# Kernel optimization log

Hardware: AMD Instinct MI355X
Metric: run time of the kernel (lower is better)

The kernel has to match this reference:

```python
import jax, jax.numpy as jnp
import numpy as np

FP16_HUGE = 65504.0  # large additive mask constant (fp16-max style, as in AF2 torch ports)

B, N, T = 1, 384, 4
CQ, CT = 128, 64      # query (pair) channels, template pair channels
H = 4                 # num heads
D = CT // H           # per-head key/value dim = 16 (AF2: key_dim=value_dim=64 split over 4 heads)


def setup_inputs() -> dict:
    key = jax.random.key(0)
    ks = jax.random.split(key, 8)
    inp = {
        "query_embedding": jax.random.normal(ks[0], (B, N, N, CQ), jnp.float32),
        "template_pair_representation": jax.random.normal(ks[1], (B, T, N, N, CT), jnp.float32),
        "template_mask": jnp.ones((B, T), jnp.float32),
        # attention params (gating=False for template pointwise attention in AF2)
        "query_w": jax.random.normal(ks[2], (H, CQ, D), jnp.float32) * (CQ ** -0.5),
        "key_w": jax.random.normal(ks[3], (H, CT, D), jnp.float32) * (CT ** -0.5),
        "value_w": jax.random.normal(ks[4], (H, CT, D), jnp.float32) * (CT ** -0.5),
        "output_w": jax.random.normal(ks[5], (H, D, CQ), jnp.float32) * ((H * D) ** -0.5),
        "output_b": jnp.zeros((CQ,), jnp.float32),
    }
    return inp


def reference(query_embedding, template_pair_representation, template_mask,
              query_w, key_w, value_w, output_w, output_b):
    b, n, _, cq = query_embedding.shape
    t = template_mask.shape[-1]
    d = query_w.shape[-1]

    # [b, n*n, 1, cq]: each (i,j) pair position attends over templates
    flat_q = query_embedding.reshape(b, n * n, 1, cq)
    # [b, t, n, n, ct] -> [b, n, n, t, ct] -> [b, n*n, t, ct]
    flat_t = jnp.transpose(template_pair_representation, (0, 2, 3, 1, 4)).reshape(b, n * n, t, -1)

    # additive bias over key axis: 0 where mask=1, -FP16_HUGE where mask=0; [b,1,1,1,t]
    bias = FP16_HUGE * (template_mask[:, None, None, None, :] - 1.0)

    q = jnp.einsum('bpic,hcd->bphid', flat_q, query_w) * (d ** -0.5)  # [b,p,h,1,d]
    k = jnp.einsum('bptc,hcd->bphtd', flat_t, key_w)                  # [b,p,h,t,d]
    v = jnp.einsum('bptc,hcd->bphtd', flat_t, value_w)

    logits = jnp.einsum('bphid,bphtd->bphit', q, k) + bias            # [b,p,h,1,t]
    weights = jax.nn.softmax(logits, axis=-1)
    wv = jnp.einsum('bphit,bphtd->bphid', weights, v)                 # [b,p,h,1,d]
    out = jnp.einsum('bphid,hdc->bpic', wv, output_w) + output_b      # [b,p,1,cq]

    embedding = out.reshape(b, n, n, cq)
    tmask = (jnp.sum(template_mask.reshape(b, -1), axis=1) > 0.0).astype(embedding.dtype)
    return embedding * tmask[:, None, None, None]
```

## Files before the change

### kernel.cpp

```cpp
#include <hip/hip_runtime.h>
#include <hip/hip_bf16.h>

typedef __attribute__((ext_vector_type(8))) short bf16x8;
typedef __attribute__((ext_vector_type(4))) float f32x4;
typedef unsigned int u32;
typedef unsigned short u16;

#define NPOS 147456
#define NTILES 9216
#define NBLK 1536
#define ITERS 6

__device__ inline u16 bfc(float f) {
  union { __hip_bfloat16 h; u16 s; } u;
  u.h = __float2bfloat16(f);
  return u.s;
}

__global__ void prep_kernel(const float* __restrict__ wq, const float* __restrict__ wk,
                            const float* __restrict__ wv, const float* __restrict__ wo,
                            u16* __restrict__ wsf) {
  int gid = blockIdx.x * 256 + threadIdx.x;
  int idx, which;
  if (gid < 8192)       { idx = gid;         which = 0; }
  else if (gid < 12288) { idx = gid - 8192;  which = 1; }
  else if (gid < 16384) { idx = gid - 12288; which = 2; }
  else                  { idx = gid - 16384; which = 3; }
  int fragid = idx >> 9, lane = (idx >> 3) & 63, e = idx & 7;
  int l15 = lane & 15, g = lane >> 4;
  float v;
  if (which == 0) {
    int n = fragid >> 2, kc = fragid & 3;
    int c = kc * 32 + g * 8 + e;
    v = wq[n * 2048 + c * 16 + l15] * 0.25f;
  } else if (which == 1) {
    int n = fragid >> 1, kc = fragid & 1;
    int c = kc * 32 + g * 8 + e;
    v = wk[n * 1024 + c * 16 + l15];
  } else if (which == 2) {
    int n = fragid >> 1, kc = fragid & 1;
    int c = kc * 32 + g * 8 + e;
    v = wv[n * 1024 + c * 16 + l15];
  } else {
    int n8 = fragid >> 1, kc = fragid & 1;
    int hd = kc * 32 + g * 8 + e;
    v = wo[(hd >> 4) * 2048 + (hd & 15) * 128 + n8 * 16 + l15];
  }
  wsf[gid] = bfc(v);
}

#define WQF(n, kc)  ((((n) * 4 + (kc))) * 64)
#define WKF(n, kc)  ((16 + (n) * 2 + (kc)) * 64)
#define WVF(n, kc)  ((24 + (n) * 2 + (kc)) * 64)
#define WOF(n8, kc) ((32 + (n8) * 2 + (kc)) * 64)

typedef const __attribute__((address_space(1))) u32 gas_u32;
typedef __attribute__((address_space(3))) u32 las_u32;

#define STR2_(x) #x
#define WAITVM(n) asm volatile("s_waitcnt vmcnt(" STR2_(n) ")" ::: "memory")
#define SBAR      __builtin_amdgcn_s_barrier()
#define SCHB      __builtin_amdgcn_sched_barrier(0)
#define WAITLGKM  asm volatile("s_waitcnt lgkmcnt(0)" ::: "memory")

__global__ __launch_bounds__(256) void tpa_kernel(
    const float* __restrict__ qe, const float* __restrict__ tpr,
    const float* __restrict__ tmk_p, const float* __restrict__ ob,
    const u16* __restrict__ wsf, float* __restrict__ out)
{
  __shared__ int4 qls4[512];
  __shared__ int4 thA4[512];
  __shared__ int4 thB4[512];
  __shared__ u32 wvsh32[512];
  char* const qls  = (char*)qls4;
  char* const thA  = (char*)thA4;
  char* const thB  = (char*)thB4;
  char* const wvsh = (char*)wvsh32;

  const int tid = threadIdx.x;
  const int wid = tid >> 6;
  const int lane = tid & 63;
  const int l15 = lane & 15, g = lane >> 4;
  const int swz = (l15 & 7) << 4;
  const int h = wid;

  const char* qdb[2];
  #pragma unroll
  for (int j = 0; j < 2; ++j) {
    int m = (wid * 2 + j) * 64 + lane;
    int pos = m >> 5, c16 = m & 31;
    qdb[j] = (const char*)qe + (size_t)pos * 512 + ((c16 * 16) ^ ((pos & 7) << 4));
  }
  const char* tdb[2][2];
  #pragma unroll
  for (int hf = 0; hf < 2; ++hf)
    #pragma unroll
    for (int j = 0; j < 2; ++j) {
      int m = (wid * 2 + j) * 64 + lane;
      int t = hf * 2 + (m >> 8), pos = (m >> 4) & 15, c16 = m & 15;
      tdb[hf][j] = (const char*)tpr + ((size_t)t * NPOS + pos) * 256 +
                   ((c16 * 16) ^ ((pos & 7) << 4));
    }

#define STAGE_Q(P)                                                             \
  { _Pragma("unroll") for (int j = 0; j < 2; ++j) {                            \
      const char* s_ = qdb[j] + (size_t)(P) * 512;                             \
      char* d_ = qls + (wid * 2 + j) * 1024;                                   \
      __builtin_amdgcn_global_load_lds((gas_u32*)s_, (las_u32*)d_, 16, 0, 0); } }

#define STAGE_T(HF, DST, P)                                                    \
  { _Pragma("unroll") for (int j = 0; j < 2; ++j) {                            \
      const char* s_ = tdb[HF][j] + (size_t)(P) * 256;                         \
      char* d_ = (DST) + (wid * 2 + j) * 1024;                                 \
      __builtin_amdgcn_global_load_lds((gas_u32*)s_, (las_u32*)d_, 16, 0, 0); } }

  const bf16x8* wf = (const bf16x8*)wsf;
  bf16x8 wqf[4], wkf[2], wvf[2], wof[2][2];
  #pragma unroll
  for (int kc = 0; kc < 4; ++kc) wqf[kc] = wf[WQF(h, kc) + lane];
  #pragma unroll
  for (int kc = 0; kc < 2; ++kc) {
    wkf[kc] = wf[WKF(h, kc) + lane];
    wvf[kc] = wf[WVF(h, kc) + lane];
    wof[0][kc] = wf[WOF(2 * h + 0, kc) + lane];
    wof[1][kc] = wf[WOF(2 * h + 1, kc) + lane];
  }

  const float m0 = tmk_p[0], m1 = tmk_p[1], m2 = tmk_p[2], m3 = tmk_p[3];
  const float biasv[4] = {65504.0f * (m0 - 1.0f), 65504.0f * (m1 - 1.0f),
                          65504.0f * (m2 - 1.0f), 65504.0f * (m3 - 1.0f)};
  const float tmk = (m0 + m1 + m2 + m3 > 0.0f) ? 1.0f : 0.0f;

  f32x4 obf[2];
  {
    const f32x4* obase = reinterpret_cast<const f32x4*>(ob);
    #pragma unroll
    for (int j = 0; j < 2; ++j) {
      const f32x4 o = obase[(2 * h + j) * 4 + g];
      #pragma unroll
      for (int r = 0; r < 4; ++r) obf[j][r] = o[r] * tmk;
    }
  }

  SCHB;
  STAGE_Q(blockIdx.x * 16)
  STAGE_T(0, thA, blockIdx.x * 16)
  STAGE_T(1, thB, blockIdx.x * 16)
  SCHB;

#define TSTEP(TROW, BIAS)                                                      \
  { bf16x8 at0, at1;                                                           \
    { f32x4 lo = *(const f32x4*)((TROW) + ((g * 32) ^ swz));                   \
      f32x4 hi = *(const f32x4*)((TROW) + ((g * 32 + 16) ^ swz));              \
      _Pragma("unroll")                                                        \
      for (int e = 0; e < 4; ++e) { at0[e] = (short)bfc(lo[e]); at0[e + 4] = (short)bfc(hi[e]); } } \
    { f32x4 lo = *(const f32x4*)((TROW) + ((128 + g * 32) ^ swz));             \
      f32x4 hi = *(const f32x4*)((TROW) + ((128 + g * 32 + 16) ^ swz));        \
      _Pragma("unroll")                                                        \
      for (int e = 0; e < 4; ++e) { at1[e] = (short)bfc(lo[e]); at1[e + 4] = (short)bfc(hi[e]); } } \
    f32x4 kT = (f32x4){0.f, 0.f, 0.f, 0.f};                                    \
    f32x4 vT = (f32x4){0.f, 0.f, 0.f, 0.f};                                    \
    kT = __builtin_amdgcn_mfma_f32_16x16x32_bf16(wkf[0], at0, kT, 0, 0, 0);    \
    kT = __builtin_amdgcn_mfma_f32_16x16x32_bf16(wkf[1], at1, kT, 0, 0, 0);    \
    vT = __builtin_amdgcn_mfma_f32_16x16x32_bf16(wvf[0], at0, vT, 0, 0, 0);    \
    vT = __builtin_amdgcn_mfma_f32_16x16x32_bf16(wvf[1], at1, vT, 0, 0, 0);    \
    float lg = qT[0] * kT[0] + qT[1] * kT[1] + qT[2] * kT[2] + qT[3] * kT[3];  \
    lg += __shfl_xor(lg, 16);                                                  \
    lg += __shfl_xor(lg, 32);                                                  \
    const float w = __expf(lg + (BIAS));                                       \
    ssum += w;                                                                 \
    _Pragma("unroll")                                                          \
    for (int r = 0; r < 4; ++r) wvT[r] += w * vT[r]; }

#define BODY(IT, WNA)                                                          \
{                                                                              \
  const int it_ = (IT);                                                        \
  const int p0 = (blockIdx.x + it_ * NBLK) * 16;                               \
  const int np0 = (blockIdx.x + ((it_ + 1 < ITERS) ? it_ + 1 : it_) * NBLK) * 16; \
                                                    \
  SCHB; WAITVM(WNA); SBAR; SCHB;                                               \
  f32x4 qT = (f32x4){0.f, 0.f, 0.f, 0.f};                                      \
  { const char* qrow = qls + l15 * 512;                                        \
    _Pragma("unroll")                                                          \
    for (int kc = 0; kc < 4; ++kc) {                                           \
      const int cb = kc * 128 + g * 32;                                        \
      f32x4 lo = *(const f32x4*)(qrow + ((cb) ^ swz));                         \
      f32x4 hi = *(const f32x4*)(qrow + ((cb + 16) ^ swz));                    \
      bf16x8 aq;                                                               \
      _Pragma("unroll")                                                        \
      for (int e = 0; e < 4; ++e) { aq[e] = (short)bfc(lo[e]); aq[e + 4] = (short)bfc(hi[e]); } \
      qT = __builtin_amdgcn_mfma_f32_16x16x32_bf16(wqf[kc], aq, qT, 0, 0, 0);  \
    } }                                                                        \
  float ssum = 0.f;                                                            \
  f32x4 wvT = (f32x4){0.f, 0.f, 0.f, 0.f};                                     \
  TSTEP(thA + 0 * 4096 + l15 * 256, biasv[0])                                  \
  TSTEP(thA + 1 * 4096 + l15 * 256, biasv[1])                                  \
                                 \
  SCHB; WAITLGKM; SBAR; SCHB;                                                  \
  STAGE_Q(np0)                                                                 \
  STAGE_T(0, thA, np0)                                                         \
                                                        \
  SCHB; WAITVM(4); SBAR; SCHB;                                                 \
  TSTEP(thB + 0 * 4096 + l15 * 256, biasv[2])                                  \
  TSTEP(thB + 1 * 4096 + l15 * 256, biasv[3])                                  \
  { const float inv = tmk / fmaxf(ssum, 1e-30f);                               \
    u32 pk0 = (u32)bfc(wvT[0] * inv) | ((u32)bfc(wvT[1] * inv) << 16);         \
    u32 pk1 = (u32)bfc(wvT[2] * inv) | ((u32)bfc(wvT[3] * inv) << 16);         \
    const int hb = h * 32 + g * 8;                                             \
    *(u32*)(wvsh + ((l15 * 128 + hb) ^ swz))     = pk0;                        \
    *(u32*)(wvsh + ((l15 * 128 + hb + 4) ^ swz)) = pk1; }                      \
                                             \
  SCHB; WAITLGKM; SBAR; SCHB;                                                  \
  { bf16x8 bwv0 = *(const bf16x8*)(wvsh + ((l15 * 128 + g * 16)      ^ swz));  \
    bf16x8 bwv1 = *(const bf16x8*)(wvsh + ((l15 * 128 + 64 + g * 16) ^ swz));  \
    _Pragma("unroll")                                                          \
    for (int j = 0; j < 2; ++j) {                                              \
      f32x4 acc = (f32x4){0.f, 0.f, 0.f, 0.f};                                 \
      acc = __builtin_amdgcn_mfma_f32_16x16x32_bf16(wof[j][0], bwv0, acc, 0, 0, 0); \
      acc = __builtin_amdgcn_mfma_f32_16x16x32_bf16(wof[j][1], bwv1, acc, 0, 0, 0); \
      f32x4 res;                                                               \
      _Pragma("unroll")                                                        \
      for (int r = 0; r < 4; ++r) res[r] = acc[r] + obf[j][r];                 \
      *(f32x4*)(out + (size_t)(p0 + l15) * 128 + (2 * h + j) * 16 + g * 4) = res; \
    } }                                                                        \
  SCHB;                                                                        \
  STAGE_T(1, thB, np0)                                                         \
  SCHB;                                                                        \
}

  BODY(0, 2)
  #pragma unroll 1
  for (int it = 1; it < ITERS; ++it) {
    BODY(it, 4)
  }
}

extern "C" void kernel_launch(void* const* d_in, const int* in_sizes, int n_in,
                              void* d_out, int out_size, void* d_ws, size_t ws_size,
                              hipStream_t stream) {
  const float* qe  = (const float*)d_in[0];
  const float* tpr = (const float*)d_in[1];
  const float* tmk = (const float*)d_in[2];
  const float* wq  = (const float*)d_in[3];
  const float* wk  = (const float*)d_in[4];
  const float* wv  = (const float*)d_in[5];
  const float* wo  = (const float*)d_in[6];
  const float* ob  = (const float*)d_in[7];
  float* out = (float*)d_out;
  u16* wsf = (u16*)d_ws;

  prep_kernel<<<96, 256, 0, stream>>>(wq, wk, wv, wo, wsf);
  tpa_kernel<<<NBLK, 256, 0, stream>>>(qe, tpr, tmk, ob, wsf, out);
}
```

Before: 61.53 us.

## Process two 16-position tiles per block iteration and halve the grid

Each block now handles two 16-position tiles per iteration with duplicated LDS buffers, interleaving their Q GEMMs, template steps and output GEMMs. The grid is halved so each block covers 32 positions per iteration with the same iteration count. The aim is to amortize barriers and waits over twice the work and to expose more independent MFMA and load work for latency hiding. In exchange LDS use per block doubles, register pressure rises, and fewer blocks are resident, which may lower occupancy.

```diff
diff --git a/kernel.cpp b/kernel.cpp
--- a/kernel.cpp
+++ b/kernel.cpp
@@ -8,7 +8,7 @@
 
 #define NPOS 147456
 #define NTILES 9216
-#define NBLK 1536
+#define NBLK 768
 #define ITERS 6
 
 __device__ inline u16 bfc(float f) {
@@ -68,14 +68,14 @@
     const float* __restrict__ tmk_p, const float* __restrict__ ob,
     const u16* __restrict__ wsf, float* __restrict__ out)
 {
-  __shared__ int4 qls4[512];
-  __shared__ int4 thA4[512];
-  __shared__ int4 thB4[512];
-  __shared__ u32 wvsh32[512];
-  char* const qls  = (char*)qls4;
-  char* const thA  = (char*)thA4;
-  char* const thB  = (char*)thB4;
-  char* const wvsh = (char*)wvsh32;
+  __shared__ int4 qls4[2][512];
+  __shared__ int4 thA4[2][512];
+  __shared__ int4 thB4[2][512];
+  __shared__ u32 wvsh32[2][512];
+  char* const qls0 = (char*)qls4[0];   char* const qls1 = (char*)qls4[1];
+  char* const thA0 = (char*)thA4[0];   char* const thA1 = (char*)thA4[1];
+  char* const thB0 = (char*)thB4[0];   char* const thB1 = (char*)thB4[1];
+  char* const exc0 = (char*)wvsh32[0]; char* const exc1 = (char*)wvsh32[1];
 
   const int tid = threadIdx.x;
   const int wid = tid >> 6;
@@ -102,10 +102,10 @@
                    ((c16 * 16) ^ ((pos & 7) << 4));
     }
 
-#define STAGE_Q(P)                                                             \
+#define STAGE_Q(DST, P)                                                        \
   { _Pragma("unroll") for (int j = 0; j < 2; ++j) {                            \
       const char* s_ = qdb[j] + (size_t)(P) * 512;                             \
-      char* d_ = qls + (wid * 2 + j) * 1024;                                   \
+      char* d_ = (DST) + (wid * 2 + j) * 1024;                                 \
       __builtin_amdgcn_global_load_lds((gas_u32*)s_, (las_u32*)d_, 16, 0, 0); } }
 
 #define STAGE_T(HF, DST, P)                                                    \
@@ -143,12 +143,28 @@
   }
 
   SCHB;
-  STAGE_Q(blockIdx.x * 16)
-  STAGE_T(0, thA, blockIdx.x * 16)
-  STAGE_T(1, thB, blockIdx.x * 16)
+  STAGE_Q(qls0, blockIdx.x * 32)
+  STAGE_T(0, thA0, blockIdx.x * 32)
+  STAGE_Q(qls1, blockIdx.x * 32 + 16)
+  STAGE_T(0, thA1, blockIdx.x * 32 + 16)
+  STAGE_T(1, thB0, blockIdx.x * 32)
+  STAGE_T(1, thB1, blockIdx.x * 32 + 16)
   SCHB;
 
-#define TSTEP(TROW, BIAS)                                                      \
+#define QGEMM(QT, QBUF)                                                        \
+  { const char* qrow = (QBUF) + l15 * 512;                                     \
+    _Pragma("unroll")                                                          \
+    for (int kc = 0; kc < 4; ++kc) {                                           \
+      const int cb = kc * 128 + g * 32;                                        \
+      f32x4 lo = *(const f32x4*)(qrow + ((cb) ^ swz));                         \
+      f32x4 hi = *(const f32x4*)(qrow + ((cb + 16) ^ swz));                    \
+      bf16x8 aq;                                                               \
+      _Pragma("unroll")                                                        \
+      for (int e = 0; e < 4; ++e) { aq[e] = (short)bfc(lo[e]); aq[e + 4] = (short)bfc(hi[e]); } \
+      QT = __builtin_amdgcn_mfma_f32_16x16x32_bf16(wqf[kc], aq, QT, 0, 0, 0);  \
+    } }
+
+#define TSTEP(TROW, BIAS, QT, SSUM, WVT)                                       \
   { bf16x8 at0, at1;                                                           \
     { f32x4 lo = *(const f32x4*)((TROW) + ((g * 32) ^ swz));                   \
       f32x4 hi = *(const f32x4*)((TROW) + ((g * 32 + 16) ^ swz));              \
@@ -164,55 +180,25 @@
     kT = __builtin_amdgcn_mfma_f32_16x16x32_bf16(wkf[1], at1, kT, 0, 0, 0);    \
     vT = __builtin_amdgcn_mfma_f32_16x16x32_bf16(wvf[0], at0, vT, 0, 0, 0);    \
     vT = __builtin_amdgcn_mfma_f32_16x16x32_bf16(wvf[1], at1, vT, 0, 0, 0);    \
-    float lg = qT[0] * kT[0] + qT[1] * kT[1] + qT[2] * kT[2] + qT[3] * kT[3];  \
+    float lg = (QT)[0] * kT[0] + (QT)[1] * kT[1] + (QT)[2] * kT[2] + (QT)[3] * kT[3]; \
     lg += __shfl_xor(lg, 16);                                                  \
     lg += __shfl_xor(lg, 32);                                                  \
     const float w = __expf(lg + (BIAS));                                       \
-    ssum += w;                                                                 \
+    (SSUM) += w;                                                               \
     _Pragma("unroll")                                                          \
-    for (int r = 0; r < 4; ++r) wvT[r] += w * vT[r]; }
-
-#define BODY(IT, WNA)                                                          \
-{                                                                              \
-  const int it_ = (IT);                                                        \
-  const int p0 = (blockIdx.x + it_ * NBLK) * 16;                               \
-  const int np0 = (blockIdx.x + ((it_ + 1 < ITERS) ? it_ + 1 : it_) * NBLK) * 16; \
-                                                    \
-  SCHB; WAITVM(WNA); SBAR; SCHB;                                               \
-  f32x4 qT = (f32x4){0.f, 0.f, 0.f, 0.f};                                      \
-  { const char* qrow = qls + l15 * 512;                                        \
-    _Pragma("unroll")                                                          \
-    for (int kc = 0; kc < 4; ++kc) {                                           \
-      const int cb = kc * 128 + g * 32;                                        \
-      f32x4 lo = *(const f32x4*)(qrow + ((cb) ^ swz));                         \
-      f32x4 hi = *(const f32x4*)(qrow + ((cb + 16) ^ swz));                    \
-      bf16x8 aq;                                                               \
-      _Pragma("unroll")                                                        \
-      for (int e = 0; e < 4; ++e) { aq[e] = (short)bfc(lo[e]); aq[e + 4] = (short)bfc(hi[e]); } \
-      qT = __builtin_amdgcn_mfma_f32_16x16x32_bf16(wqf[kc], aq, qT, 0, 0, 0);  \
-    } }                                                                        \
-  float ssum = 0.f;                                                            \
-  f32x4 wvT = (f32x4){0.f, 0.f, 0.f, 0.f};                                     \
-  TSTEP(thA + 0 * 4096 + l15 * 256, biasv[0])                                  \
-  TSTEP(thA + 1 * 4096 + l15 * 256, biasv[1])                                  \
-                                 \
-  SCHB; WAITLGKM; SBAR; SCHB;                                                  \
-  STAGE_Q(np0)                                                                 \
-  STAGE_T(0, thA, np0)                                                         \
-                                                        \
-  SCHB; WAITVM(4); SBAR; SCHB;                                                 \
-  TSTEP(thB + 0 * 4096 + l15 * 256, biasv[2])                                  \
-  TSTEP(thB + 1 * 4096 + l15 * 256, biasv[3])                                  \
-  { const float inv = tmk / fmaxf(ssum, 1e-30f);                               \
-    u32 pk0 = (u32)bfc(wvT[0] * inv) | ((u32)bfc(wvT[1] * inv) << 16);         \
-    u32 pk1 = (u32)bfc(wvT[2] * inv) | ((u32)bfc(wvT[3] * inv) << 16);         \
+    for (int r = 0; r < 4; ++r) (WVT)[r] += w * vT[r]; }
+
+#define PACK(EXB, SSUM, WVT)                                                   \
+  { const float inv = tmk / fmaxf((SSUM), 1e-30f);                             \
+    u32 pk0 = (u32)bfc((WVT)[0] * inv) | ((u32)bfc((WVT)[1] * inv) << 16);     \
+    u32 pk1 = (u32)bfc((WVT)[2] * inv) | ((u32)bfc((WVT)[3] * inv) << 16);     \
     const int hb = h * 32 + g * 8;                                             \
-    *(u32*)(wvsh + ((l15 * 128 + hb) ^ swz))     = pk0;                        \
-    *(u32*)(wvsh + ((l15 * 128 + hb + 4) ^ swz)) = pk1; }                      \
-                                             \
-  SCHB; WAITLGKM; SBAR; SCHB;                                                  \
-  { bf16x8 bwv0 = *(const bf16x8*)(wvsh + ((l15 * 128 + g * 16)      ^ swz));  \
-    bf16x8 bwv1 = *(const bf16x8*)(wvsh + ((l15 * 128 + 64 + g * 16) ^ swz));  \
+    *(u32*)((EXB) + ((l15 * 128 + hb) ^ swz))     = pk0;                       \
+    *(u32*)((EXB) + ((l15 * 128 + hb + 4) ^ swz)) = pk1; }
+
+#define OUTG(EXB, P0)                                                          \
+  { bf16x8 bwv0 = *(const bf16x8*)((EXB) + ((l15 * 128 + g * 16)      ^ swz)); \
+    bf16x8 bwv1 = *(const bf16x8*)((EXB) + ((l15 * 128 + 64 + g * 16) ^ swz)); \
     _Pragma("unroll")                                                          \
     for (int j = 0; j < 2; ++j) {                                              \
       f32x4 acc = (f32x4){0.f, 0.f, 0.f, 0.f};                                 \
@@ -221,17 +207,55 @@
       f32x4 res;                                                               \
       _Pragma("unroll")                                                        \
       for (int r = 0; r < 4; ++r) res[r] = acc[r] + obf[j][r];                 \
-      *(f32x4*)(out + (size_t)(p0 + l15) * 128 + (2 * h + j) * 16 + g * 4) = res; \
-    } }                                                                        \
+      *(f32x4*)(out + (size_t)((P0) + l15) * 128 + (2 * h + j) * 16 + g * 4) = res; \
+    } }
+
+#define BODY(IT, WN1)                                                          \
+{                                                                              \
+  const int it_ = (IT);                                                        \
+  const int pr = blockIdx.x + it_ * NBLK;                                      \
+  const int pA = pr * 32, pB = pr * 32 + 16;                                   \
+  const int nr = blockIdx.x + ((it_ + 1 < ITERS) ? it_ + 1 : it_) * NBLK;      \
+  const int nA = nr * 32, nB = nr * 32 + 16;                                   \
+                                     \
+  SCHB; WAITVM(WN1); SBAR; SCHB;                                               \
+  f32x4 qTA = (f32x4){0.f, 0.f, 0.f, 0.f};                                     \
+  f32x4 qTB = (f32x4){0.f, 0.f, 0.f, 0.f};                                     \
+  QGEMM(qTA, qls0)                                                             \
+  QGEMM(qTB, qls1)                                                             \
+  float ssA = 0.f, ssB = 0.f;                                                  \
+  f32x4 wvA = (f32x4){0.f, 0.f, 0.f, 0.f};                                     \
+  f32x4 wvB = (f32x4){0.f, 0.f, 0.f, 0.f};                                     \
+  TSTEP(thA0 + 0 * 4096 + l15 * 256, biasv[0], qTA, ssA, wvA)                  \
+  TSTEP(thA1 + 0 * 4096 + l15 * 256, biasv[0], qTB, ssB, wvB)                  \
+  TSTEP(thA0 + 1 * 4096 + l15 * 256, biasv[1], qTA, ssA, wvA)                  \
+  TSTEP(thA1 + 1 * 4096 + l15 * 256, biasv[1], qTB, ssB, wvB)                  \
+                                \
+  SCHB; WAITLGKM; SBAR; SCHB;                                                  \
+  STAGE_Q(qls0, nA) STAGE_T(0, thA0, nA)                                       \
+  STAGE_Q(qls1, nB) STAGE_T(0, thA1, nB)                                       \
+                                         \
+  SCHB; WAITVM(8); SBAR; SCHB;                                                 \
+  TSTEP(thB0 + 0 * 4096 + l15 * 256, biasv[2], qTA, ssA, wvA)                  \
+  TSTEP(thB1 + 0 * 4096 + l15 * 256, biasv[2], qTB, ssB, wvB)                  \
+  TSTEP(thB0 + 1 * 4096 + l15 * 256, biasv[3], qTA, ssA, wvA)                  \
+  TSTEP(thB1 + 1 * 4096 + l15 * 256, biasv[3], qTB, ssB, wvB)                  \
+  PACK(exc0, ssA, wvA)                                                         \
+  PACK(exc1, ssB, wvB)                                                         \
+                                            \
+  SCHB; WAITLGKM; SBAR; SCHB;                                                  \
+  OUTG(exc0, pA)                                                               \
+  OUTG(exc1, pB)                                                               \
   SCHB;                                                                        \
-  STAGE_T(1, thB, np0)                                                         \
+  STAGE_T(1, thB0, nA)                                                         \
+  STAGE_T(1, thB1, nB)                                                         \
   SCHB;                                                                        \
 }
 
-  BODY(0, 2)
+  BODY(0, 4)
   #pragma unroll 1
   for (int it = 1; it < ITERS; ++it) {
-    BODY(it, 4)
+    BODY(it, 8)
   }
 }
 
```

After: 67.75 us. +10.1%, slower.
